# Kernel optimization log

Hardware: AMD Instinct MI355X
Metric: run time of the kernel (lower is better)

Reference implementation:

```python
import jax, jax.numpy as jnp
import numpy as np

N_VARS = 1_000_000
NB, NS, NL = 400_000, 300_000, 200_000  # binary / small-int / large-int counts
C_CLS = 16
N_CON = 500_000
E = 16_000_000
LP_SOL_COL = 8
BIAS_COL = 1
LAMBDA_MEAN, LAMBDA_MAX = 1.0, 0.1


def setup_inputs() -> dict:
    key = jax.random.key(0)
    ks = jax.random.split(key, 10)
    # disjoint variable index partitions: [0,NB) bin, [NB,NB+NS) small int,
    # [NB+NS,NB+NS+NL) large int, rest continuous (var_types==0)
    idx_bin = jnp.arange(NB, dtype=jnp.int64)
    idx_int_small = jnp.arange(NB, NB + NS, dtype=jnp.int64)
    idx_int_large = jnp.arange(NB + NS, NB + NS + NL, dtype=jnp.int64)
    var_types = jnp.concatenate([
        jnp.ones(NB, dtype=jnp.int64),                 # binary
        jnp.full((NS + NL,), 2, dtype=jnp.int64),      # integer
        jnp.zeros(N_VARS - NB - NS - NL, dtype=jnp.int64),  # continuous
    ])
    edge_indices = jnp.stack([
        jax.random.randint(ks[0], (E,), 0, N_CON, dtype=jnp.int64),
        jax.random.randint(ks[1], (E,), 0, N_VARS, dtype=jnp.int64),
    ])
    return {
        'prob_bin': jax.random.uniform(ks[2], (NB, 1), jnp.float32),
        'logits_int_small': jax.random.normal(ks[3], (NS, C_CLS), jnp.float32),
        'int_small_offsets': jax.random.normal(ks[4], (NS,), jnp.float32),
        'pred_int_large': jax.random.normal(ks[5], (NL, 1), jnp.float32),
        'edge_features': jax.random.normal(ks[6], (E, 1), jnp.float32),
        'constraint_features': jax.random.normal(ks[7], (N_CON, 8), jnp.float32),
        'variable_features': jax.random.normal(ks[8], (N_VARS, 16), jnp.float32),
        'idx_bin': idx_bin,
        'idx_int_small': idx_int_small,
        'idx_int_large': idx_int_large,
        'var_types': var_types,
        'edge_indices': edge_indices,
        'n_vars': N_VARS,
    }


def _build_x(prob_bin, logits_int_small, int_small_offsets, pred_int_large,
             variable_features, idx_bin, idx_int_small, idx_int_large,
             var_types, n_vars):
    x = jnp.zeros((n_vars,), dtype=prob_bin.dtype)
    x = x.at[idx_bin].set(prob_bin[:, 0])
    # expected value of small-int class distribution
    probs = jax.nn.softmax(logits_int_small, axis=-1)                  # [NS, C]
    class_values = jnp.arange(logits_int_small.shape[1], dtype=probs.dtype)
    expected = probs @ class_values + int_small_offsets                # [NS]
    x = x.at[idx_int_small].set(expected)
    x = x.at[idx_int_large].set(pred_int_large[:, 0])
    # continuous vars take detached LP solution values
    lp_vals = jax.lax.stop_gradient(variable_features[:, LP_SOL_COL])
    x = jnp.where(var_types == 0, lp_vals, x)
    return x


def reference(prob_bin, logits_int_small, int_small_offsets, pred_int_large,
              edge_features, constraint_features, variable_features,
              idx_bin, idx_int_small, idx_int_large, var_types,
              edge_indices, n_vars):
    x = _build_x(prob_bin, logits_int_small, int_small_offsets, pred_int_large,
                 variable_features, idx_bin, idx_int_small, idx_int_large,
                 var_types, n_vars)
    n_cons = constraint_features.shape[0]
    # sparse A @ x: gather variable values along edges, scale, scatter-add per constraint
    weighted = edge_features.reshape(-1) * x[edge_indices[1]]          # [E]
    Ax = jax.ops.segment_sum(weighted, edge_indices[0], num_segments=n_cons)
    violation = jax.nn.relu(Ax - constraint_features[:, BIAS_COL])     # [N_con]
    mean_viol = violation.mean()
    max_viol = violation.max()
    n_violated = jnp.sum(violation > 1e-6)
    penalty = LAMBDA_MEAN * mean_viol + LAMBDA_MAX * max_viol
    return penalty, mean_viol, max_viol, n_violated
```

## Files before the change

kernel.cpp:

```cpp
#include <hip/hip_runtime.h>


#define BSHIFT 14
#define BROWS  (1 << BSHIFT)
#define NBUCK_MAX 32
#define CHUNK 8192
#define ROUNDS (CHUNK / 1024)
#define BUF 128
#define THRESH 48
#define SPLIT 8

typedef int      iv4 __attribute__((ext_vector_type(4)));
typedef float    fv4 __attribute__((ext_vector_type(4)));
typedef unsigned uv4 __attribute__((ext_vector_type(4)));

__device__ inline unsigned bf16bits(float v) {
    unsigned f = __float_as_uint(v);
    return (f + 0x7FFFu + ((f >> 16) & 1u)) >> 16;
}
__device__ inline float bf16val(unsigned bits) {
    return __uint_as_float(bits << 16);
}


__global__ __launch_bounds__(256) void k_build_hist(
    const int* __restrict__ rows, int* __restrict__ counts, int nchunks, int gHist,
    const float* __restrict__ prob_bin, const int* __restrict__ idx_bin, int NB, int gBin,
    const float* __restrict__ logits, const float* __restrict__ offs,
    const int* __restrict__ idx_small, int NS, int gSml,
    const float* __restrict__ pred, const int* __restrict__ idx_large, int NL, int gLrg,
    const int* __restrict__ vt, const float* __restrict__ vf, int NV,
    int E, int nbuck, unsigned short* __restrict__ xb, float* __restrict__ acc)
{
    int blk = blockIdx.x, tid = threadIdx.x;
    if (blk == 0 && tid < 4) reinterpret_cast<unsigned*>(acc)[tid] = 0u;

    if (blk < gHist) {
        __shared__ int h[4][NBUCK_MAX];
        int wid = tid >> 6, lane = tid & 63;
        if (lane < NBUCK_MAX) h[wid][lane] = 0;
        __syncthreads();
        int e4max = E >> 2;
        int b4 = blk * (CHUNK / 4);
#pragma unroll
        for (int k = 0; k < ROUNDS; ++k) {
            int i4 = b4 + k * 256 + tid;
            if (i4 < e4max) {
                iv4 r = __builtin_nontemporal_load(reinterpret_cast<const iv4*>(rows) + i4);
                atomicAdd(&h[wid][r.x >> BSHIFT], 1);
                atomicAdd(&h[wid][r.y >> BSHIFT], 1);
                atomicAdd(&h[wid][r.z >> BSHIFT], 1);
                atomicAdd(&h[wid][r.w >> BSHIFT], 1);
            }
        }
        if (blk == 0 && tid < (E & 3))
            atomicAdd(&h[wid][rows[(E & ~3) + tid] >> BSHIFT], 1);
        __syncthreads();
        if (tid < nbuck)
            counts[(size_t)tid * nchunks + blk] =
                h[0][tid] + h[1][tid] + h[2][tid] + h[3][tid];
        return;
    }
    blk -= gHist;
    if (blk < gBin) {
        int i = blk * 256 + tid;
        if (i < NB) xb[idx_bin[i]] = (unsigned short)bf16bits(prob_bin[i]);
        return;
    }
    blk -= gBin;
    if (blk < gSml) {
        int i = blk * 256 + tid;
        if (i < NS) {
            const fv4* lp = reinterpret_cast<const fv4*>(logits + (size_t)i * 16);
            fv4 v0 = lp[0], v1 = lp[1], v2 = lp[2], v3 = lp[3];
            float l[16] = {v0.x, v0.y, v0.z, v0.w, v1.x, v1.y, v1.z, v1.w,
                           v2.x, v2.y, v2.z, v2.w, v3.x, v3.y, v3.z, v3.w};
            float m = l[0];
#pragma unroll
            for (int j = 1; j < 16; ++j) m = fmaxf(m, l[j]);
            float s = 0.f, ws = 0.f;
#pragma unroll
            for (int j = 0; j < 16; ++j) {
                float e = expf(l[j] - m);
                s += e;
                ws += e * (float)j;
            }
            xb[idx_small[i]] = (unsigned short)bf16bits(ws / s + offs[i]);
        }
        return;
    }
    blk -= gSml;
    if (blk < gLrg) {
        int i = blk * 256 + tid;
        if (i < NL) xb[idx_large[i]] = (unsigned short)bf16bits(pred[i]);
        return;
    }
    blk -= gLrg;
    {
        int v = blk * 256 + tid;
        if (v < NV && vt[v] == 0) xb[v] = (unsigned short)bf16bits(vf[(size_t)v * 16 + 8]);
    }
}


__global__ __launch_bounds__(1024) void k_scan(const int* __restrict__ counts,
                                               int* __restrict__ off,
                                               int* __restrict__ total, int nchunks) {
    int b = blockIdx.x;
    __shared__ int wtot[16];
    __shared__ int wbase[16];
    int tid = threadIdx.x, w = tid >> 6, lane = tid & 63;
    int seg = (nchunks + 15) >> 4;
    int lo = w * seg;
    int hi = lo + seg; if (hi > nchunks) hi = nchunks;
    const int* cb = counts + (size_t)b * nchunks;
    int* ob = off + (size_t)b * nchunks;
    int carry = 0;
    for (int i0 = lo; i0 < hi; i0 += 64) {
        int i = i0 + lane;
        int v = (i < hi) ? cb[i] : 0;
        int orig = v;
#pragma unroll
        for (int o = 1; o < 64; o <<= 1) {
            int t = __shfl_up(v, o, 64);
            if (lane >= o) v += t;
        }
        if (i < hi) ob[i] = carry + v - orig;
        carry += __shfl(v, 63, 64);
    }
    if (lane == 0) wtot[w] = carry;
    __syncthreads();
    if (tid == 0) {
        int s = 0;
        for (int k = 0; k < 16; ++k) { wbase[k] = s; s += wtot[k]; }
        total[b] = s;
    }
    __syncthreads();
    int add = wbase[w];
    if (add)
        for (int i = lo + lane; i < hi; i += 64) ob[i] += add;
}


__global__ __launch_bounds__(256) void k_scatter6(const int* __restrict__ rows,
                                                  const int* __restrict__ cols,
                                                  const float* __restrict__ ef,
                                                  const unsigned short* __restrict__ xb,
                                                  const int* __restrict__ off,
                                                  const int* __restrict__ total,
                                                  unsigned* __restrict__ recs,
                                                  int nchunks, int E, int nbuck) {
    __shared__ unsigned bufr[NBUCK_MAX][BUF];
    __shared__ int fill[NBUCK_MAX];
    __shared__ int done[NBUCK_MAX];
    __shared__ int cbase[NBUCK_MAX];

    int tid = threadIdx.x, chunk = blockIdx.x, wid = tid >> 6, lane = tid & 63;
    if (tid < 32) {
        int t = (tid < nbuck) ? total[tid] : 0;
        int p = (t + 3) & ~3;
        int sc = p;
#pragma unroll
        for (int o = 1; o < 32; o <<= 1) {
            int u = __shfl_up(sc, o, 64);
            if (tid >= o) sc += u;
        }
        cbase[tid] = (sc - p) + ((tid < nbuck) ? off[(size_t)tid * nchunks + chunk] : 0);
        fill[tid] = 0;
        done[tid] = 0;
    }
    __syncthreads();

    int e4max = E >> 2;
    int b4 = chunk * (CHUNK / 4);

    iv4 rA, cA; fv4 fA; bool vA;
    iv4 rB, cB; fv4 fB; bool vB;
    unsigned gA0, gA1, gA2, gA3, gB0, gB1, gB2, gB3;

#define LOADK(k, R, C, F, V)                                                   \
    {   int i4 = b4 + (k) * 256 + tid;                                         \
        V = i4 < e4max;                                                        \
        if (V) {                                                               \
            R = __builtin_nontemporal_load(reinterpret_cast<const iv4*>(rows) + i4); \
            C = __builtin_nontemporal_load(reinterpret_cast<const iv4*>(cols) + i4); \
            F = __builtin_nontemporal_load(reinterpret_cast<const fv4*>(ef) + i4);   \
        } }
#define GATHK(C, V, G0, G1, G2, G3)                                            \
    if (V) { G0 = xb[C.x]; G1 = xb[C.y]; G2 = xb[C.z]; G3 = xb[C.w]; }

    LOADK(0, rA, cA, fA, vA)
    GATHK(cA, vA, gA0, gA1, gA2, gA3)

    for (int k = 0; k < ROUNDS; ++k) {
        if (k + 1 < ROUNDS) {
            LOADK(k + 1, rB, cB, fB, vB)
            GATHK(cB, vB, gB0, gB1, gB2, gB3)
        }
        if (vA) {
            unsigned q[4] = {bf16bits(fA.x * bf16val(gA0)),
                             bf16bits(fA.y * bf16val(gA1)),
                             bf16bits(fA.z * bf16val(gA2)),
                             bf16bits(fA.w * bf16val(gA3))};
            int ra[4] = {rA.x, rA.y, rA.z, rA.w};
#pragma unroll
            for (int j = 0; j < 4; ++j) {
                int b = ra[j] >> BSHIFT;
                unsigned rec = ((unsigned)(ra[j] & (BROWS - 1)) << 16) | q[j];
                int pos = atomicAdd(&fill[b], 1);
                if (pos < BUF) bufr[b][pos] = rec;
                else recs[cbase[b] + done[b] + pos] = rec;
            }
        }
        if (k == ROUNDS - 1 && chunk == 0 && tid < (E & 3)) {
            int e = (E & ~3) + tid;
            int rrow = rows[e];
            unsigned rec = ((unsigned)(rrow & (BROWS - 1)) << 16)
                         | bf16bits(ef[e] * bf16val(xb[cols[e]]));
            int b = rrow >> BSHIFT;
            int pos = atomicAdd(&fill[b], 1);
            if (pos < BUF) bufr[b][pos] = rec;
            else recs[cbase[b] + done[b] + pos] = rec;
        }
        __syncthreads();
        bool last = (k == ROUNDS - 1);
        for (int b = wid; b < nbuck; b += 4) {
            int fl = fill[b];
            if (fl == 0) continue;
            if (fl >= THRESH || last) {
                int n = fl < BUF ? fl : BUF;
                int g = cbase[b] + done[b];
                for (int j = lane; j < n; j += 64)
                    __builtin_nontemporal_store(bufr[b][j], recs + g + j);
                if (lane == 0) { done[b] += fl; fill[b] = 0; }
            }
        }
        __syncthreads();
        rA = rB; cA = cB; fA = fB; vA = vB;
        gA0 = gB0; gA1 = gB1; gA2 = gB2; gA3 = gB3;
    }
#undef LOADK
#undef GATHK
}


__global__ __launch_bounds__(256) void k_accum(const unsigned* __restrict__ recs,
                                               const int* __restrict__ total,
                                               float* __restrict__ partial, int nbuck) {
    __shared__ float tile[BROWS];
    __shared__ int sb[2];
    int tid = threadIdx.x;
    int b = blockIdx.x / SPLIT, s = blockIdx.x % SPLIT;
    if (tid < 32) {
        int t = (tid < nbuck) ? total[tid] : 0;
        int pq = (t + 3) & ~3;
        int sc = pq;
#pragma unroll
        for (int o = 1; o < 32; o <<= 1) {
            int u = __shfl_up(sc, o, 64);
            if (tid >= o) sc += u;
        }
        if (tid == b) { sb[0] = sc - pq; sb[1] = t; }
    }
    fv4 z = {0.f, 0.f, 0.f, 0.f};
    for (int i = tid; i < BROWS / 4; i += 256) reinterpret_cast<fv4*>(tile)[i] = z;
    __syncthreads();
    int lo = sb[0], len = sb[1], hi = lo + len;
    int per = ((len + SPLIT - 1) / SPLIT + 3) & ~3;
    int s0 = lo + s * per;
    int s1 = s0 + per; if (s1 > hi) s1 = hi;
    int i = s0 + (tid << 2);
    for (; i + 3 < s1; i += 1024) {
        uv4 r = __builtin_nontemporal_load(reinterpret_cast<const uv4*>(recs + i));
        atomicAdd(&tile[r.x >> 16], __uint_as_float((r.x & 0xFFFFu) << 16));
        atomicAdd(&tile[r.y >> 16], __uint_as_float((r.y & 0xFFFFu) << 16));
        atomicAdd(&tile[r.z >> 16], __uint_as_float((r.z & 0xFFFFu) << 16));
        atomicAdd(&tile[r.w >> 16], __uint_as_float((r.w & 0xFFFFu) << 16));
    }
    if (i < s1)
        for (int j = i; j < s1; ++j) {
            unsigned rr = recs[j];
            atomicAdd(&tile[rr >> 16], __uint_as_float((rr & 0xFFFFu) << 16));
        }
    __syncthreads();
    float* out = partial + ((size_t)blockIdx.x << BSHIFT);
    for (int j = tid; j < BROWS / 4; j += 256)
        __builtin_nontemporal_store(reinterpret_cast<const fv4*>(tile)[j],
                                    reinterpret_cast<fv4*>(out) + j);
}


__global__ __launch_bounds__(256) void k_reduce_fin(const float* __restrict__ partial,
                                                    const float* __restrict__ cf,
                                                    float* __restrict__ acc,
                                                    float* __restrict__ out,
                                                    int ncon, int nblocks) {
    float lsum = 0.f, lmax = 0.f;
    unsigned lcnt = 0;
    int stride = gridDim.x * blockDim.x;
    for (int c = blockIdx.x * blockDim.x + threadIdx.x; c < ncon; c += stride) {
        int b = c >> BSHIFT, i = c & (BROWS - 1);
        const float* p = partial + (((size_t)b * SPLIT) << BSHIFT) + i;
        float v = 0.f;
#pragma unroll
        for (int s = 0; s < SPLIT; ++s)
            v += __builtin_nontemporal_load(p + ((size_t)s << BSHIFT));
        v -= cf[(size_t)c * 8 + 1];
        v = v > 0.f ? v : 0.f;
        lsum += v;
        lmax = fmaxf(lmax, v);
        lcnt += (v > 1e-6f) ? 1u : 0u;
    }
#pragma unroll
    for (int o = 32; o > 0; o >>= 1) {
        lsum += __shfl_down(lsum, o);
        lmax = fmaxf(lmax, __shfl_down(lmax, o));
        lcnt += __shfl_down(lcnt, o);
    }
    __shared__ float ssum[4];
    __shared__ float smax[4];
    __shared__ unsigned scnt[4];
    int lane = threadIdx.x & 63, wid = threadIdx.x >> 6;
    if (lane == 0) { ssum[wid] = lsum; smax[wid] = lmax; scnt[wid] = lcnt; }
    __syncthreads();
    if (threadIdx.x == 0) {
        float bs = 0.f, bm = 0.f;
        unsigned bc = 0;
        for (int w = 0; w < 4; ++w) { bs += ssum[w]; bm = fmaxf(bm, smax[w]); bc += scnt[w]; }
        atomicAdd(&acc[0], bs);
        atomicMax(reinterpret_cast<unsigned*>(acc) + 1, __float_as_uint(bm));
        atomicAdd(reinterpret_cast<unsigned*>(acc) + 2, bc);
        __threadfence();
        unsigned t = atomicAdd(reinterpret_cast<unsigned*>(acc) + 3, 1u);
        if (t == (unsigned)(nblocks - 1)) {
            float sum   = atomicAdd(&acc[0], 0.f);
            unsigned mb = atomicMax(reinterpret_cast<unsigned*>(acc) + 1, 0u);
            unsigned ct = atomicAdd(reinterpret_cast<unsigned*>(acc) + 2, 0u);
            float mean = sum / (float)ncon;
            float mx = __uint_as_float(mb);
            out[0] = mean + 0.1f * mx;
            out[1] = mean;
            out[2] = mx;
            out[3] = (float)ct;
        }
    }
}


__global__ void k_edges(const float* __restrict__ ef, const int* __restrict__ rows,
                        const int* __restrict__ cols, const unsigned short* __restrict__ xb,
                        float* __restrict__ Ax, int e4, int E) {
    int stride = gridDim.x * blockDim.x;
    int gid = blockIdx.x * blockDim.x + threadIdx.x;
    for (int i = gid; i < e4; i += stride) {
        fv4 f = reinterpret_cast<const fv4*>(ef)[i];
        iv4 r = reinterpret_cast<const iv4*>(rows)[i];
        iv4 c = reinterpret_cast<const iv4*>(cols)[i];
        atomicAdd(&Ax[r.x], f.x * bf16val(xb[c.x]));
        atomicAdd(&Ax[r.y], f.y * bf16val(xb[c.y]));
        atomicAdd(&Ax[r.z], f.z * bf16val(xb[c.z]));
        atomicAdd(&Ax[r.w], f.w * bf16val(xb[c.w]));
    }
    for (int e = e4 * 4 + gid; e < E; e += stride)
        atomicAdd(&Ax[rows[e]], ef[e] * bf16val(xb[cols[e]]));
}

__global__ void k_reduce_ax(const float* __restrict__ Ax, const float* __restrict__ cf,
                            float* __restrict__ acc, float* __restrict__ out,
                            int ncon, int nblocks) {
    float lsum = 0.f, lmax = 0.f;
    unsigned lcnt = 0;
    int stride = gridDim.x * blockDim.x;
    for (int c = blockIdx.x * blockDim.x + threadIdx.x; c < ncon; c += stride) {
        float v = Ax[c] - cf[(size_t)c * 8 + 1];
        v = v > 0.f ? v : 0.f;
        lsum += v;
        lmax = fmaxf(lmax, v);
        lcnt += (v > 1e-6f) ? 1u : 0u;
    }
#pragma unroll
    for (int o = 32; o > 0; o >>= 1) {
        lsum += __shfl_down(lsum, o);
        lmax = fmaxf(lmax, __shfl_down(lmax, o));
        lcnt += __shfl_down(lcnt, o);
    }
    __shared__ float ssum[4];
    __shared__ float smax[4];
    __shared__ unsigned scnt[4];
    int lane = threadIdx.x & 63, wid = threadIdx.x >> 6;
    if (lane == 0) { ssum[wid] = lsum; smax[wid] = lmax; scnt[wid] = lcnt; }
    __syncthreads();
    if (threadIdx.x == 0) {
        float bs = 0.f, bm = 0.f;
        unsigned bc = 0;
        for (int w = 0; w < 4; ++w) { bs += ssum[w]; bm = fmaxf(bm, smax[w]); bc += scnt[w]; }
        atomicAdd(&acc[0], bs);
        atomicMax(reinterpret_cast<unsigned*>(acc) + 1, __float_as_uint(bm));
        atomicAdd(reinterpret_cast<unsigned*>(acc) + 2, bc);
        __threadfence();
        unsigned t = atomicAdd(reinterpret_cast<unsigned*>(acc) + 3, 1u);
        if (t == (unsigned)(nblocks - 1)) {
            float sum   = atomicAdd(&acc[0], 0.f);
            unsigned mb = atomicMax(reinterpret_cast<unsigned*>(acc) + 1, 0u);
            unsigned ct = atomicAdd(reinterpret_cast<unsigned*>(acc) + 2, 0u);
            float mean = sum / (float)ncon;
            float mx = __uint_as_float(mb);
            out[0] = mean + 0.1f * mx;
            out[1] = mean;
            out[2] = mx;
            out[3] = (float)ct;
        }
    }
}


extern "C" void kernel_launch(void* const* d_in, const int* in_sizes, int n_in,
                              void* d_out, int out_size, void* d_ws, size_t ws_size,
                              hipStream_t stream) {
    const float* prob_bin     = (const float*)d_in[0];
    const float* logits_small = (const float*)d_in[1];
    const float* offs_small   = (const float*)d_in[2];
    const float* pred_large   = (const float*)d_in[3];
    const float* edge_feat    = (const float*)d_in[4];
    const float* cons_feat    = (const float*)d_in[5];
    const float* var_feat     = (const float*)d_in[6];
    const int*   idx_bin      = (const int*)d_in[7];
    const int*   idx_small    = (const int*)d_in[8];
    const int*   idx_large    = (const int*)d_in[9];
    const int*   var_types    = (const int*)d_in[10];
    const int*   edge_indices = (const int*)d_in[11];

    const int NB    = in_sizes[0];
    const int NS    = in_sizes[2];
    const int NL    = in_sizes[3];
    const int E     = in_sizes[4];
    const int NCON  = in_sizes[5] / 8;
    const int NVARS = in_sizes[10];

    const int* rows = edge_indices;
    const int* cols = edge_indices + E;

    const int nbuck   = (NCON + BROWS - 1) >> BSHIFT;
    const int nchunks = (E + CHUNK - 1) / CHUNK;

    char* w = (char*)d_ws;
    size_t o = 0;
    auto take = [&](size_t bytes) -> char* {
        char* p = w + o;
        o = (o + bytes + 255) & ~(size_t)255;
        return p;
    };
    unsigned short* xb = (unsigned short*)take((size_t)NVARS * 2);
    unsigned* recs     = (unsigned*)take((size_t)(E + 4 * NBUCK_MAX) * 4);
    float*    partial  = (float*)take((size_t)nbuck * SPLIT * BROWS * 4);
    int*      counts   = (int*)take((size_t)nbuck * nchunks * 4);
    int*      off      = (int*)take((size_t)nbuck * nchunks * 4);
    int*      total    = (int*)take((size_t)nbuck * 4);
    float*    acc      = (float*)take(32);
    size_t need = o;

    const int B = 256;
    bool sorted_path = (ws_size >= need) && (nbuck <= NBUCK_MAX);

    const int gBin = (NB + B - 1) / B;
    const int gSml = (NS + B - 1) / B;
    const int gLrg = (NL + B - 1) / B;
    const int gCnt = (NVARS + B - 1) / B;

    if (sorted_path) {
        k_build_hist<<<nchunks + gBin + gSml + gLrg + gCnt, B, 0, stream>>>(
            rows, counts, nchunks, nchunks,
            prob_bin, idx_bin, NB, gBin,
            logits_small, offs_small, idx_small, NS, gSml,
            pred_large, idx_large, NL, gLrg,
            var_types, var_feat, NVARS,
            E, nbuck, xb, acc);
        k_scan<<<nbuck, 1024, 0, stream>>>(counts, off, total, nchunks);
        k_scatter6<<<nchunks, B, 0, stream>>>(rows, cols, edge_feat, xb, off, total,
                                              recs, nchunks, E, nbuck);
        k_accum<<<nbuck * SPLIT, B, 0, stream>>>(recs, total, partial, nbuck);
        const int rblocks = 1024;
        k_reduce_fin<<<rblocks, B, 0, stream>>>(partial, cons_feat, acc, (float*)d_out,
                                                NCON, rblocks);
    } else {
        float* accf = (float*)((char*)d_ws + (((size_t)NVARS * 2 + 255) & ~(size_t)255));
        float* Ax   = accf + 8;
        (void)hipMemsetAsync(accf, 0, (size_t)(8 + NCON) * sizeof(float), stream);
        k_build_hist<<<gBin + gSml + gLrg + gCnt, B, 0, stream>>>(
            rows, counts, nchunks, 0,
            prob_bin, idx_bin, NB, gBin,
            logits_small, offs_small, idx_small, NS, gSml,
            pred_large, idx_large, NL, gLrg,
            var_types, var_feat, NVARS,
            E, nbuck, xb, accf);
        k_edges<<<2048, B, 0, stream>>>(edge_feat, rows, cols, xb, Ax, E / 4, E);
        k_reduce_ax<<<1024, B, 0, stream>>>(Ax, cons_feat, accf, (float*)d_out, NCON, 1024);
    }
}
```

Baseline: 274.5 us.

## Replace histogram+scan bucketing with atomic per-shard bucket cursors and overflow atomics

Removes the histogram pass over the row indices and the prefix-scan kernel. Edges are now binned into fixed-capacity per-bucket, per-shard record regions whose write positions come from global atomic cursors. Any overflow past the shared buffer or region capacity is accumulated directly into a global Ax array with float atomics, which k_accum adds back in. This drops one full read of the rows array and two kernel launches, at the cost of global atomic contention, a memset, and a nondeterministic record order. The shared-memory buffer and flush threshold are also enlarged.

```diff
diff --git a/kernel.cpp b/kernel.cpp
--- a/kernel.cpp
+++ b/kernel.cpp
@@ -6,8 +6,8 @@
 #define NBUCK_MAX 32
 #define CHUNK 8192
 #define ROUNDS (CHUNK / 1024)
-#define BUF 128
-#define THRESH 48
+#define BUF 192
+#define THRESH 96
 #define SPLIT 8
 
 typedef int      iv4 __attribute__((ext_vector_type(4)));
@@ -23,45 +23,18 @@
 }
 
 
-__global__ __launch_bounds__(256) void k_build_hist(
-    const int* __restrict__ rows, int* __restrict__ counts, int nchunks, int gHist,
+__global__ __launch_bounds__(256) void k_build_x(
     const float* __restrict__ prob_bin, const int* __restrict__ idx_bin, int NB, int gBin,
     const float* __restrict__ logits, const float* __restrict__ offs,
     const int* __restrict__ idx_small, int NS, int gSml,
     const float* __restrict__ pred, const int* __restrict__ idx_large, int NL, int gLrg,
     const int* __restrict__ vt, const float* __restrict__ vf, int NV,
-    int E, int nbuck, unsigned short* __restrict__ xb, float* __restrict__ acc)
+    unsigned short* __restrict__ xb, int* __restrict__ ctl, int nctl)
 {
     int blk = blockIdx.x, tid = threadIdx.x;
-    if (blk == 0 && tid < 4) reinterpret_cast<unsigned*>(acc)[tid] = 0u;
-
-    if (blk < gHist) {
-        __shared__ int h[4][NBUCK_MAX];
-        int wid = tid >> 6, lane = tid & 63;
-        if (lane < NBUCK_MAX) h[wid][lane] = 0;
-        __syncthreads();
-        int e4max = E >> 2;
-        int b4 = blk * (CHUNK / 4);
-#pragma unroll
-        for (int k = 0; k < ROUNDS; ++k) {
-            int i4 = b4 + k * 256 + tid;
-            if (i4 < e4max) {
-                iv4 r = __builtin_nontemporal_load(reinterpret_cast<const iv4*>(rows) + i4);
-                atomicAdd(&h[wid][r.x >> BSHIFT], 1);
-                atomicAdd(&h[wid][r.y >> BSHIFT], 1);
-                atomicAdd(&h[wid][r.z >> BSHIFT], 1);
-                atomicAdd(&h[wid][r.w >> BSHIFT], 1);
-            }
-        }
-        if (blk == 0 && tid < (E & 3))
-            atomicAdd(&h[wid][rows[(E & ~3) + tid] >> BSHIFT], 1);
-        __syncthreads();
-        if (tid < nbuck)
-            counts[(size_t)tid * nchunks + blk] =
-                h[0][tid] + h[1][tid] + h[2][tid] + h[3][tid];
-        return;
-    }
-    blk -= gHist;
+    if (blk == 0)
+        for (int i = tid; i < nctl; i += 256) ctl[i] = 0;
+
     if (blk < gBin) {
         int i = blk * 256 + tid;
         if (i < NB) xb[idx_bin[i]] = (unsigned short)bf16bits(prob_bin[i]);
@@ -103,72 +76,20 @@
 }
 
 
-__global__ __launch_bounds__(1024) void k_scan(const int* __restrict__ counts,
-                                               int* __restrict__ off,
-                                               int* __restrict__ total, int nchunks) {
-    int b = blockIdx.x;
-    __shared__ int wtot[16];
-    __shared__ int wbase[16];
-    int tid = threadIdx.x, w = tid >> 6, lane = tid & 63;
-    int seg = (nchunks + 15) >> 4;
-    int lo = w * seg;
-    int hi = lo + seg; if (hi > nchunks) hi = nchunks;
-    const int* cb = counts + (size_t)b * nchunks;
-    int* ob = off + (size_t)b * nchunks;
-    int carry = 0;
-    for (int i0 = lo; i0 < hi; i0 += 64) {
-        int i = i0 + lane;
-        int v = (i < hi) ? cb[i] : 0;
-        int orig = v;
-#pragma unroll
-        for (int o = 1; o < 64; o <<= 1) {
-            int t = __shfl_up(v, o, 64);
-            if (lane >= o) v += t;
-        }
-        if (i < hi) ob[i] = carry + v - orig;
-        carry += __shfl(v, 63, 64);
-    }
-    if (lane == 0) wtot[w] = carry;
-    __syncthreads();
-    if (tid == 0) {
-        int s = 0;
-        for (int k = 0; k < 16; ++k) { wbase[k] = s; s += wtot[k]; }
-        total[b] = s;
-    }
-    __syncthreads();
-    int add = wbase[w];
-    if (add)
-        for (int i = lo + lane; i < hi; i += 64) ob[i] += add;
-}
-
-
-__global__ __launch_bounds__(256) void k_scatter6(const int* __restrict__ rows,
+__global__ __launch_bounds__(256) void k_scatter7(const int* __restrict__ rows,
                                                   const int* __restrict__ cols,
                                                   const float* __restrict__ ef,
                                                   const unsigned short* __restrict__ xb,
-                                                  const int* __restrict__ off,
-                                                  const int* __restrict__ total,
+                                                  int* __restrict__ gcur8,
                                                   unsigned* __restrict__ recs,
-                                                  int nchunks, int E, int nbuck) {
+                                                  float* __restrict__ Axg,
+                                                  int E, int nbuck, int C8) {
     __shared__ unsigned bufr[NBUCK_MAX][BUF];
     __shared__ int fill[NBUCK_MAX];
-    __shared__ int done[NBUCK_MAX];
-    __shared__ int cbase[NBUCK_MAX];
 
     int tid = threadIdx.x, chunk = blockIdx.x, wid = tid >> 6, lane = tid & 63;
-    if (tid < 32) {
-        int t = (tid < nbuck) ? total[tid] : 0;
-        int p = (t + 3) & ~3;
-        int sc = p;
-#pragma unroll
-        for (int o = 1; o < 32; o <<= 1) {
-            int u = __shfl_up(sc, o, 64);
-            if (tid >= o) sc += u;
-        }
-        cbase[tid] = (sc - p) + ((tid < nbuck) ? off[(size_t)tid * nchunks + chunk] : 0);
-        fill[tid] = 0;
-        done[tid] = 0;
-    }
+    int shard = chunk & (SPLIT - 1);
+    if (tid < NBUCK_MAX) fill[tid] = 0;
     __syncthreads();
 
     int e4max = E >> 2;
@@ -198,29 +119,27 @@
             GATHK(cB, vB, gB0, gB1, gB2, gB3)
         }
         if (vA) {
-            unsigned q[4] = {bf16bits(fA.x * bf16val(gA0)),
-                             bf16bits(fA.y * bf16val(gA1)),
-                             bf16bits(fA.z * bf16val(gA2)),
-                             bf16bits(fA.w * bf16val(gA3))};
+            float pf[4] = {fA.x * bf16val(gA0), fA.y * bf16val(gA1),
+                           fA.z * bf16val(gA2), fA.w * bf16val(gA3)};
             int ra[4] = {rA.x, rA.y, rA.z, rA.w};
 #pragma unroll
             for (int j = 0; j < 4; ++j) {
                 int b = ra[j] >> BSHIFT;
-                unsigned rec = ((unsigned)(ra[j] & (BROWS - 1)) << 16) | q[j];
+                unsigned rec = ((unsigned)(ra[j] & (BROWS - 1)) << 16) | bf16bits(pf[j]);
                 int pos = atomicAdd(&fill[b], 1);
                 if (pos < BUF) bufr[b][pos] = rec;
-                else recs[cbase[b] + done[b] + pos] = rec;
+                else atomicAdd(&Axg[ra[j]], pf[j]);
             }
         }
         if (k == ROUNDS - 1 && chunk == 0 && tid < (E & 3)) {
             int e = (E & ~3) + tid;
             int rrow = rows[e];
-            unsigned rec = ((unsigned)(rrow & (BROWS - 1)) << 16)
-                         | bf16bits(ef[e] * bf16val(xb[cols[e]]));
+            float pv = ef[e] * bf16val(xb[cols[e]]);
             int b = rrow >> BSHIFT;
+            unsigned rec = ((unsigned)(rrow & (BROWS - 1)) << 16) | bf16bits(pv);
             int pos = atomicAdd(&fill[b], 1);
             if (pos < BUF) bufr[b][pos] = rec;
-            else recs[cbase[b] + done[b] + pos] = rec;
+            else atomicAdd(&Axg[rrow], pv);
         }
         __syncthreads();
         bool last = (k == ROUNDS - 1);
@@ -229,10 +148,20 @@
             if (fl == 0) continue;
             if (fl >= THRESH || last) {
                 int n = fl < BUF ? fl : BUF;
-                int g = cbase[b] + done[b];
-                for (int j = lane; j < n; j += 64)
-                    __builtin_nontemporal_store(bufr[b][j], recs + g + j);
-                if (lane == 0) { done[b] += fl; fill[b] = 0; }
+                int pos;
+                if (lane == 0) pos = atomicAdd(&gcur8[b * SPLIT + shard], n);
+                pos = __shfl(pos, 0);
+                unsigned* reg = recs + (size_t)(b * SPLIT + shard) * C8;
+                for (int j = lane; j < n; j += 64) {
+                    unsigned rec = bufr[b][j];
+                    int idx = pos + j;
+                    if (idx < C8)
+                        __builtin_nontemporal_store(rec, reg + idx);
+                    else
+                        atomicAdd(&Axg[(b << BSHIFT) | (int)(rec >> 16)],
+                                  bf16val(rec & 0xFFFFu));
+                }
+                if (lane == 0) fill[b] = 0;
             }
         }
         __syncthreads();
@@ -245,43 +174,34 @@
 
 
 __global__ __launch_bounds__(256) void k_accum(const unsigned* __restrict__ recs,
-                                               const int* __restrict__ total,
-                                               float* __restrict__ partial, int nbuck) {
+                                               const int* __restrict__ gcur8,
+                                               const float* __restrict__ Axg,
+                                               float* __restrict__ partial, int C8) {
     __shared__ float tile[BROWS];
-    __shared__ int sb[2];
     int tid = threadIdx.x;
     int b = blockIdx.x / SPLIT, s = blockIdx.x % SPLIT;
-    if (tid < 32) {
-        int t = (tid < nbuck) ? total[tid] : 0;
-        int pq = (t + 3) & ~3;
-        int sc = pq;
-#pragma unroll
-        for (int o = 1; o < 32; o <<= 1) {
-            int u = __shfl_up(sc, o, 64);
-            if (tid >= o) sc += u;
-        }
-        if (tid == b) { sb[0] = sc - pq; sb[1] = t; }
-    }
     fv4 z = {0.f, 0.f, 0.f, 0.f};
     for (int i = tid; i < BROWS / 4; i += 256) reinterpret_cast<fv4*>(tile)[i] = z;
     __syncthreads();
-    int lo = sb[0], len = sb[1], hi = lo + len;
-    int per = ((len + SPLIT - 1) / SPLIT + 3) & ~3;
-    int s0 = lo + s * per;
-    int s1 = s0 + per; if (s1 > hi) s1 = hi;
-    int i = s0 + (tid << 2);
-    for (; i + 3 < s1; i += 1024) {
-        uv4 r = __builtin_nontemporal_load(reinterpret_cast<const uv4*>(recs + i));
+    int len = gcur8[b * SPLIT + s];
+    if (len > C8) len = C8;
+    const unsigned* rp = recs + (size_t)(b * SPLIT + s) * C8;
+    for (int i = tid << 2; i + 3 < len; i += 1024) {
+        uv4 r = __builtin_nontemporal_load(reinterpret_cast<const uv4*>(rp + i));
         atomicAdd(&tile[r.x >> 16], __uint_as_float((r.x & 0xFFFFu) << 16));
         atomicAdd(&tile[r.y >> 16], __uint_as_float((r.y & 0xFFFFu) << 16));
         atomicAdd(&tile[r.z >> 16], __uint_as_float((r.z & 0xFFFFu) << 16));
         atomicAdd(&tile[r.w >> 16], __uint_as_float((r.w & 0xFFFFu) << 16));
     }
-    if (i < s1)
-        for (int j = i; j < s1; ++j) {
-            unsigned rr = recs[j];
-            atomicAdd(&tile[rr >> 16], __uint_as_float((rr & 0xFFFFu) << 16));
-        }
+    if (tid < (len & 3)) {
+        unsigned rr = rp[(len & ~3) + tid];
+        atomicAdd(&tile[rr >> 16], __uint_as_float((rr & 0xFFFFu) << 16));
+    }
+    __syncthreads();
+    if (s == 0) {
+        const float* ax = Axg + ((size_t)b << BSHIFT);
+        for (int i = tid; i < BROWS; i += 256) tile[i] += ax[i];
+    }
     __syncthreads();
     float* out = partial + ((size_t)blockIdx.x << BSHIFT);
     for (int j = tid; j < BROWS / 4; j += 256)
@@ -443,6 +363,9 @@
     const int nbuck   = (NCON + BROWS - 1) >> BSHIFT;
     const int nchunks = (E + CHUNK - 1) / CHUNK;
 
+    int c8 = (nbuck > 0) ? (int)(((long long)E * 3) / (2LL * nbuck * SPLIT)) : 0;
+    c8 = (c8 + 1024 + 3) & ~3;
+
     char* w = (char*)d_ws;
     size_t o = 0;
     auto take = [&](size_t bytes) -> char* {
@@ -451,13 +374,15 @@
         return p;
     };
     unsigned short* xb = (unsigned short*)take((size_t)NVARS * 2);
-    unsigned* recs     = (unsigned*)take((size_t)(E + 4 * NBUCK_MAX) * 4);
+    unsigned* recs     = (unsigned*)take((size_t)nbuck * SPLIT * c8 * 4);
     float*    partial  = (float*)take((size_t)nbuck * SPLIT * BROWS * 4);
-    int*      counts   = (int*)take((size_t)nbuck * nchunks * 4);
-    int*      off      = (int*)take((size_t)nbuck * nchunks * 4);
-    int*      total    = (int*)take((size_t)nbuck * 4);
-    float*    acc      = (float*)take(32);
+    float*    Axg      = (float*)take((size_t)nbuck * BROWS * 4);
+    int*      ctl      = (int*)take((NBUCK_MAX * SPLIT + 4) * 4);
     size_t need = o;
+
+    int*   gcur8 = ctl;
+    float* acc   = (float*)(ctl + NBUCK_MAX * SPLIT);
+    const int NCTL = NBUCK_MAX * SPLIT + 4;
 
     const int B = 256;
     bool sorted_path = (ws_size >= need) && (nbuck <= NBUCK_MAX);
@@ -468,17 +393,15 @@
     const int gCnt = (NVARS + B - 1) / B;
 
     if (sorted_path) {
-        k_build_hist<<<nchunks + gBin + gSml + gLrg + gCnt, B, 0, stream>>>(
-            rows, counts, nchunks, nchunks,
+        (void)hipMemsetAsync(Axg, 0, (size_t)nbuck * BROWS * 4, stream);
+        k_build_x<<<gBin + gSml + gLrg + gCnt, B, 0, stream>>>(
             prob_bin, idx_bin, NB, gBin,
             logits_small, offs_small, idx_small, NS, gSml,
             pred_large, idx_large, NL, gLrg,
-            var_types, var_feat, NVARS,
-            E, nbuck, xb, acc);
-        k_scan<<<nbuck, 1024, 0, stream>>>(counts, off, total, nchunks);
-        k_scatter6<<<nchunks, B, 0, stream>>>(rows, cols, edge_feat, xb, off, total,
-                                              recs, nchunks, E, nbuck);
-        k_accum<<<nbuck * SPLIT, B, 0, stream>>>(recs, total, partial, nbuck);
+            var_types, var_feat, NVARS, xb, ctl, NCTL);
+        k_scatter7<<<nchunks, B, 0, stream>>>(rows, cols, edge_feat, xb, gcur8,
+                                              recs, Axg, E, nbuck, c8);
+        k_accum<<<nbuck * SPLIT, B, 0, stream>>>(recs, gcur8, Axg, partial, c8);
         const int rblocks = 1024;
         k_reduce_fin<<<rblocks, B, 0, stream>>>(partial, cons_feat, acc, (float*)d_out,
                                                 NCON, rblocks);
@@ -486,13 +409,11 @@
         float* accf = (float*)((char*)d_ws + (((size_t)NVARS * 2 + 255) & ~(size_t)255));
         float* Ax   = accf + 8;
         (void)hipMemsetAsync(accf, 0, (size_t)(8 + NCON) * sizeof(float), stream);
-        k_build_hist<<<gBin + gSml + gLrg + gCnt, B, 0, stream>>>(
-            rows, counts, nchunks, 0,
+        k_build_x<<<gBin + gSml + gLrg + gCnt, B, 0, stream>>>(
             prob_bin, idx_bin, NB, gBin,
             logits_small, offs_small, idx_small, NS, gSml,
             pred_large, idx_large, NL, gLrg,
-            var_types, var_feat, NVARS,
-            E, nbuck, xb, accf);
+            var_types, var_feat, NVARS, xb, (int*)accf, 4);
         k_edges<<<2048, B, 0, stream>>>(edge_feat, rows, cols, xb, Ax, E / 4, E);
         k_reduce_ax<<<1024, B, 0, stream>>>(Ax, cons_feat, accf, (float*)d_out, NCON, 1024);
     }
```

New measurement: 426.5 us. +55.4%, slower.

## Deepen scatter load pipeline and pre-extract constraint bias column

Applied to the files above, without the earlier changes.

The scatter kernel now prefetches edge rows, columns and features two rounds ahead in a three-slot ring, with double-buffered gathers, and fully unrolls the round loop. Its launch bounds now request an occupancy of 8 blocks per CU. The aim is to hide global load and gather latency better, at the cost of more registers. Separately, the bias column of the constraint features is copied into a contiguous array during the histogram kernel, so the final reduction reads it coalesced instead of with an 8-float stride. That copy adds some work to the first kernel.

```diff
diff --git a/kernel.cpp b/kernel.cpp
--- a/kernel.cpp
+++ b/kernel.cpp
@@ -29,7 +29,8 @@
     const float* __restrict__ logits, const float* __restrict__ offs,
     const int* __restrict__ idx_small, int NS, int gSml,
     const float* __restrict__ pred, const int* __restrict__ idx_large, int NL, int gLrg,
-    const int* __restrict__ vt, const float* __restrict__ vf, int NV,
+    const int* __restrict__ vt, const float* __restrict__ vf, int NV, int gCnt,
+    const float* __restrict__ cf, float* __restrict__ bias2, int NC,
     int E, int nbuck, unsigned short* __restrict__ xb, float* __restrict__ acc)
 {
     int blk = blockIdx.x, tid = threadIdx.x;
@@ -96,9 +97,15 @@
         return;
     }
     blk -= gLrg;
-    {
+    if (blk < gCnt) {
         int v = blk * 256 + tid;
         if (v < NV && vt[v] == 0) xb[v] = (unsigned short)bf16bits(vf[(size_t)v * 16 + 8]);
+        return;
+    }
+    blk -= gCnt;
+    {
+        int c = blk * 256 + tid;
+        if (c < NC) bias2[c] = cf[(size_t)c * 8 + 1];
     }
 }
 
@@ -142,14 +149,14 @@
 }
 
 
-__global__ __launch_bounds__(256) void k_scatter6(const int* __restrict__ rows,
-                                                  const int* __restrict__ cols,
-                                                  const float* __restrict__ ef,
-                                                  const unsigned short* __restrict__ xb,
-                                                  const int* __restrict__ off,
-                                                  const int* __restrict__ total,
-                                                  unsigned* __restrict__ recs,
-                                                  int nchunks, int E, int nbuck) {
+__global__ __launch_bounds__(256, 8) void k_scatter10(const int* __restrict__ rows,
+                                                      const int* __restrict__ cols,
+                                                      const float* __restrict__ ef,
+                                                      const unsigned short* __restrict__ xb,
+                                                      const int* __restrict__ off,
+                                                      const int* __restrict__ total,
+                                                      unsigned* __restrict__ recs,
+                                                      int nchunks, int E, int nbuck) {
     __shared__ unsigned bufr[NBUCK_MAX][BUF];
     __shared__ int fill[NBUCK_MAX];
     __shared__ int done[NBUCK_MAX];
@@ -174,39 +181,41 @@
     int e4max = E >> 2;
     int b4 = chunk * (CHUNK / 4);
 
-    iv4 rA, cA; fv4 fA; bool vA;
-    iv4 rB, cB; fv4 fB; bool vB;
-    unsigned gA0, gA1, gA2, gA3, gB0, gB1, gB2, gB3;
-
-#define LOADK(k, R, C, F, V)                                                   \
-    {   int i4 = b4 + (k) * 256 + tid;                                         \
-        V = i4 < e4max;                                                        \
-        if (V) {                                                               \
-            R = __builtin_nontemporal_load(reinterpret_cast<const iv4*>(rows) + i4); \
-            C = __builtin_nontemporal_load(reinterpret_cast<const iv4*>(cols) + i4); \
-            F = __builtin_nontemporal_load(reinterpret_cast<const fv4*>(ef) + i4);   \
+    iv4 rs[3], cs[3]; fv4 fs[3]; bool vs[3];
+    unsigned gx[2][4];
+
+#define LOADK(kk, s)                                                           \
+    {   int i4 = b4 + (kk) * 256 + tid;                                        \
+        vs[s] = i4 < e4max;                                                    \
+        if (vs[s]) {                                                           \
+            rs[s] = __builtin_nontemporal_load(reinterpret_cast<const iv4*>(rows) + i4); \
+            cs[s] = __builtin_nontemporal_load(reinterpret_cast<const iv4*>(cols) + i4); \
+            fs[s] = __builtin_nontemporal_load(reinterpret_cast<const fv4*>(ef) + i4);   \
         } }
-#define GATHK(C, V, G0, G1, G2, G3)                                            \
-    if (V) { G0 = xb[C.x]; G1 = xb[C.y]; G2 = xb[C.z]; G3 = xb[C.w]; }
-
-    LOADK(0, rA, cA, fA, vA)
-    GATHK(cA, vA, gA0, gA1, gA2, gA3)
-
+#define GATHK(s, g)                                                            \
+    if (vs[s]) {                                                               \
+        gx[g][0] = xb[cs[s].x]; gx[g][1] = xb[cs[s].y];                        \
+        gx[g][2] = xb[cs[s].z]; gx[g][3] = xb[cs[s].w];                        \
+    }
+
+    LOADK(0, 0)
+    LOADK(1, 1)
+    GATHK(0, 0)
+
+#pragma unroll
     for (int k = 0; k < ROUNDS; ++k) {
-        if (k + 1 < ROUNDS) {
-            LOADK(k + 1, rB, cB, fB, vB)
-            GATHK(cB, vB, gB0, gB1, gB2, gB3)
-        }
-        if (vA) {
-            unsigned q[4] = {bf16bits(fA.x * bf16val(gA0)),
-                             bf16bits(fA.y * bf16val(gA1)),
-                             bf16bits(fA.z * bf16val(gA2)),
-                             bf16bits(fA.w * bf16val(gA3))};
-            int ra[4] = {rA.x, rA.y, rA.z, rA.w};
+        const int s = k % 3;
+        const int g = k & 1;
+        if (k + 2 < ROUNDS) LOADK(k + 2, (k + 2) % 3)
+        if (k + 1 < ROUNDS) GATHK((k + 1) % 3, g ^ 1)
+        if (vs[s]) {
+            float pf[4] = {fs[s].x * bf16val(gx[g][0]), fs[s].y * bf16val(gx[g][1]),
+                           fs[s].z * bf16val(gx[g][2]), fs[s].w * bf16val(gx[g][3])};
+            int ra[4] = {rs[s].x, rs[s].y, rs[s].z, rs[s].w};
 #pragma unroll
             for (int j = 0; j < 4; ++j) {
                 int b = ra[j] >> BSHIFT;
-                unsigned rec = ((unsigned)(ra[j] & (BROWS - 1)) << 16) | q[j];
+                unsigned rec = ((unsigned)(ra[j] & (BROWS - 1)) << 16) | bf16bits(pf[j]);
                 int pos = atomicAdd(&fill[b], 1);
                 if (pos < BUF) bufr[b][pos] = rec;
                 else recs[cbase[b] + done[b] + pos] = rec;
@@ -223,21 +232,19 @@
             else recs[cbase[b] + done[b] + pos] = rec;
         }
         __syncthreads();
-        bool last = (k == ROUNDS - 1);
+        const bool last = (k == ROUNDS - 1);
         for (int b = wid; b < nbuck; b += 4) {
             int fl = fill[b];
             if (fl == 0) continue;
             if (fl >= THRESH || last) {
                 int n = fl < BUF ? fl : BUF;
-                int g = cbase[b] + done[b];
+                int gofs = cbase[b] + done[b];
                 for (int j = lane; j < n; j += 64)
-                    __builtin_nontemporal_store(bufr[b][j], recs + g + j);
+                    __builtin_nontemporal_store(bufr[b][j], recs + gofs + j);
                 if (lane == 0) { done[b] += fl; fill[b] = 0; }
             }
         }
         __syncthreads();
-        rA = rB; cA = cB; fA = fB; vA = vB;
-        gA0 = gB0; gA1 = gB1; gA2 = gB2; gA3 = gB3;
     }
 #undef LOADK
 #undef GATHK
@@ -291,7 +298,7 @@
 
 
 __global__ __launch_bounds__(256) void k_reduce_fin(const float* __restrict__ partial,
-                                                    const float* __restrict__ cf,
+                                                    const float* __restrict__ bias2,
                                                     float* __restrict__ acc,
                                                     float* __restrict__ out,
                                                     int ncon, int nblocks) {
@@ -305,7 +312,7 @@
 #pragma unroll
         for (int s = 0; s < SPLIT; ++s)
             v += __builtin_nontemporal_load(p + ((size_t)s << BSHIFT));
-        v -= cf[(size_t)c * 8 + 1];
+        v -= bias2[c];
         v = v > 0.f ? v : 0.f;
         lsum += v;
         lmax = fmaxf(lmax, v);
@@ -456,6 +463,7 @@
     int*      counts   = (int*)take((size_t)nbuck * nchunks * 4);
     int*      off      = (int*)take((size_t)nbuck * nchunks * 4);
     int*      total    = (int*)take((size_t)nbuck * 4);
+    float*    bias2    = (float*)take((size_t)NCON * 4);
     float*    acc      = (float*)take(32);
     size_t need = o;
 
@@ -466,21 +474,23 @@
     const int gSml = (NS + B - 1) / B;
     const int gLrg = (NL + B - 1) / B;
     const int gCnt = (NVARS + B - 1) / B;
+    const int gBia = (NCON + B - 1) / B;
 
     if (sorted_path) {
-        k_build_hist<<<nchunks + gBin + gSml + gLrg + gCnt, B, 0, stream>>>(
+        k_build_hist<<<nchunks + gBin + gSml + gLrg + gCnt + gBia, B, 0, stream>>>(
             rows, counts, nchunks, nchunks,
             prob_bin, idx_bin, NB, gBin,
             logits_small, offs_small, idx_small, NS, gSml,
             pred_large, idx_large, NL, gLrg,
-            var_types, var_feat, NVARS,
+            var_types, var_feat, NVARS, gCnt,
+            cons_feat, bias2, NCON,
             E, nbuck, xb, acc);
         k_scan<<<nbuck, 1024, 0, stream>>>(counts, off, total, nchunks);
-        k_scatter6<<<nchunks, B, 0, stream>>>(rows, cols, edge_feat, xb, off, total,
-                                              recs, nchunks, E, nbuck);
+        k_scatter10<<<nchunks, B, 0, stream>>>(rows, cols, edge_feat, xb, off, total,
+                                               recs, nchunks, E, nbuck);
         k_accum<<<nbuck * SPLIT, B, 0, stream>>>(recs, total, partial, nbuck);
         const int rblocks = 1024;
-        k_reduce_fin<<<rblocks, B, 0, stream>>>(partial, cons_feat, acc, (float*)d_out,
+        k_reduce_fin<<<rblocks, B, 0, stream>>>(partial, bias2, acc, (float*)d_out,
                                                 NCON, rblocks);
     } else {
         float* accf = (float*)((char*)d_ws + (((size_t)NVARS * 2 + 255) & ~(size_t)255));
@@ -491,7 +501,8 @@
             prob_bin, idx_bin, NB, gBin,
             logits_small, offs_small, idx_small, NS, gSml,
             pred_large, idx_large, NL, gLrg,
-            var_types, var_feat, NVARS,
+            var_types, var_feat, NVARS, gCnt,
+            cons_feat, (float*)accf, 0,
             E, nbuck, xb, accf);
         k_edges<<<2048, B, 0, stream>>>(edge_feat, rows, cols, xb, Ax, E / 4, E);
         k_reduce_ax<<<1024, B, 0, stream>>>(Ax, cons_feat, accf, (float*)d_out, NCON, 1024);
```

Measured after the change: 287.5 us. +4.8%, slower.

## Stage whole chunk's records in LDS by bucket, flush once at end

Applied to the files above, without the earlier changes.

The scatter kernel now keeps all 8192 records of a chunk in a shared-memory array. Each bucket's segment offset comes from a prefix scan of the per-chunk histogram counts. This removes the per-round flush loop, its two barriers per round, and the overflow writes straight to global memory, and replaces them with one contiguous per-bucket copy at the end. The cost is about 33KB of LDS per block, which may lower occupancy, and the global stores all happen at the end instead of overlapping with the loads.

```diff
diff --git a/kernel.cpp b/kernel.cpp
--- a/kernel.cpp
+++ b/kernel.cpp
@@ -6,8 +6,6 @@
 #define NBUCK_MAX 32
 #define CHUNK 8192
 #define ROUNDS (CHUNK / 1024)
-#define BUF 128
-#define THRESH 48
 #define SPLIT 8
 
 typedef int      iv4 __attribute__((ext_vector_type(4)));
@@ -142,17 +140,18 @@
 }
 
 
-__global__ __launch_bounds__(256) void k_scatter6(const int* __restrict__ rows,
-                                                  const int* __restrict__ cols,
-                                                  const float* __restrict__ ef,
-                                                  const unsigned short* __restrict__ xb,
-                                                  const int* __restrict__ off,
-                                                  const int* __restrict__ total,
-                                                  unsigned* __restrict__ recs,
-                                                  int nchunks, int E, int nbuck) {
-    __shared__ unsigned bufr[NBUCK_MAX][BUF];
+__global__ __launch_bounds__(256) void k_scatter11(const int* __restrict__ rows,
+                                                   const int* __restrict__ cols,
+                                                   const float* __restrict__ ef,
+                                                   const unsigned short* __restrict__ xb,
+                                                   const int* __restrict__ counts,
+                                                   const int* __restrict__ off,
+                                                   const int* __restrict__ total,
+                                                   unsigned* __restrict__ recs,
+                                                   int nchunks, int E, int nbuck) {
+    __shared__ unsigned srec[CHUNK + 4];
+    __shared__ int segb[NBUCK_MAX + 1];
     __shared__ int fill[NBUCK_MAX];
-    __shared__ int done[NBUCK_MAX];
     __shared__ int cbase[NBUCK_MAX];
 
     int tid = threadIdx.x, chunk = blockIdx.x, wid = tid >> 6, lane = tid & 63;
@@ -166,8 +165,16 @@
             if (tid >= o) sc += u;
         }
         cbase[tid] = (sc - p) + ((tid < nbuck) ? off[(size_t)tid * nchunks + chunk] : 0);
+        int c = (tid < nbuck) ? counts[(size_t)tid * nchunks + chunk] : 0;
+        int sc2 = c;
+#pragma unroll
+        for (int o = 1; o < 32; o <<= 1) {
+            int u = __shfl_up(sc2, o, 64);
+            if (tid >= o) sc2 += u;
+        }
+        segb[tid] = sc2 - c;
+        if (tid == 31) segb[32] = sc2;
         fill[tid] = 0;
-        done[tid] = 0;
     }
     __syncthreads();
 
@@ -198,49 +205,39 @@
             GATHK(cB, vB, gB0, gB1, gB2, gB3)
         }
         if (vA) {
-            unsigned q[4] = {bf16bits(fA.x * bf16val(gA0)),
-                             bf16bits(fA.y * bf16val(gA1)),
-                             bf16bits(fA.z * bf16val(gA2)),
-                             bf16bits(fA.w * bf16val(gA3))};
+            float pf[4] = {fA.x * bf16val(gA0), fA.y * bf16val(gA1),
+                           fA.z * bf16val(gA2), fA.w * bf16val(gA3)};
             int ra[4] = {rA.x, rA.y, rA.z, rA.w};
 #pragma unroll
             for (int j = 0; j < 4; ++j) {
                 int b = ra[j] >> BSHIFT;
-                unsigned rec = ((unsigned)(ra[j] & (BROWS - 1)) << 16) | q[j];
+                unsigned rec = ((unsigned)(ra[j] & (BROWS - 1)) << 16) | bf16bits(pf[j]);
                 int pos = atomicAdd(&fill[b], 1);
-                if (pos < BUF) bufr[b][pos] = rec;
-                else recs[cbase[b] + done[b] + pos] = rec;
+                srec[segb[b] + pos] = rec;
             }
         }
-        if (k == ROUNDS - 1 && chunk == 0 && tid < (E & 3)) {
-            int e = (E & ~3) + tid;
-            int rrow = rows[e];
-            unsigned rec = ((unsigned)(rrow & (BROWS - 1)) << 16)
-                         | bf16bits(ef[e] * bf16val(xb[cols[e]]));
-            int b = rrow >> BSHIFT;
-            int pos = atomicAdd(&fill[b], 1);
-            if (pos < BUF) bufr[b][pos] = rec;
-            else recs[cbase[b] + done[b] + pos] = rec;
-        }
-        __syncthreads();
-        bool last = (k == ROUNDS - 1);
-        for (int b = wid; b < nbuck; b += 4) {
-            int fl = fill[b];
-            if (fl == 0) continue;
-            if (fl >= THRESH || last) {
-                int n = fl < BUF ? fl : BUF;
-                int g = cbase[b] + done[b];
-                for (int j = lane; j < n; j += 64)
-                    __builtin_nontemporal_store(bufr[b][j], recs + g + j);
-                if (lane == 0) { done[b] += fl; fill[b] = 0; }
-            }
-        }
-        __syncthreads();
         rA = rB; cA = cB; fA = fB; vA = vB;
         gA0 = gB0; gA1 = gB1; gA2 = gB2; gA3 = gB3;
     }
+    if (chunk == 0 && tid < (E & 3)) {
+        int e = (E & ~3) + tid;
+        int rrow = rows[e];
+        unsigned rec = ((unsigned)(rrow & (BROWS - 1)) << 16)
+                     | bf16bits(ef[e] * bf16val(xb[cols[e]]));
+        int b = rrow >> BSHIFT;
+        int pos = atomicAdd(&fill[b], 1);
+        srec[segb[b] + pos] = rec;
+    }
 #undef LOADK
 #undef GATHK
+    __syncthreads();
+
+    for (int b = wid; b < nbuck; b += 4) {
+        int s0 = segb[b], n = segb[b + 1] - s0;
+        int dst = cbase[b];
+        for (int j = lane; j < n; j += 64)
+            __builtin_nontemporal_store(srec[s0 + j], recs + dst + j);
+    }
 }
 
 
@@ -476,8 +473,8 @@
             var_types, var_feat, NVARS,
             E, nbuck, xb, acc);
         k_scan<<<nbuck, 1024, 0, stream>>>(counts, off, total, nchunks);
-        k_scatter6<<<nchunks, B, 0, stream>>>(rows, cols, edge_feat, xb, off, total,
-                                              recs, nchunks, E, nbuck);
+        k_scatter11<<<nchunks, B, 0, stream>>>(rows, cols, edge_feat, xb, counts,
+                                               off, total, recs, nchunks, E, nbuck);
         k_accum<<<nbuck * SPLIT, B, 0, stream>>>(recs, total, partial, nbuck);
         const int rblocks = 1024;
         k_reduce_fin<<<rblocks, B, 0, stream>>>(partial, cons_feat, acc, (float*)d_out,
```

Result: slower. 282.1 us (+2.8%).
